# Optimization experiments

Hardware: AMD Instinct MI355X
Metric: run time of the kernel (lower is better)

The kernel has to match this reference:

```python
import jax, jax.numpy as jnp
import numpy as np

B, S, DIM = 2, 2048, 1024
EXPERT_DIM = 256
N_S, N_R, TOP_K = 2, 32, 4
EPS = 1e-6


def setup_inputs() -> dict:
    key = jax.random.key(0)
    ks = jax.random.split(key, 12)
    s1 = 1.0 / np.sqrt(DIM)        # fan-in init scale for Linear(dim, expert_dim)
    s2 = 1.0 / np.sqrt(EXPERT_DIM)  # fan-in init scale for Linear(expert_dim, dim)
    return {
        "x": jax.random.normal(ks[0], (B, S, DIM), jnp.float32),
        "rms_w": jnp.ones((DIM,), jnp.float32),
        "centroids": jax.random.normal(ks[1], (N_R, DIM), jnp.float32),
        # shared experts, stacked along leading expert axis
        "sW1": jax.random.normal(ks[2], (N_S, DIM, EXPERT_DIM), jnp.float32) * s1,
        "sb1": jax.random.normal(ks[3], (N_S, EXPERT_DIM), jnp.float32) * s1,
        "sW2": jax.random.normal(ks[4], (N_S, EXPERT_DIM, DIM), jnp.float32) * s2,
        "sb2": jax.random.normal(ks[5], (N_S, DIM), jnp.float32) * s2,
        # routed experts
        "rW1": jax.random.normal(ks[6], (N_R, DIM, EXPERT_DIM), jnp.float32) * s1,
        "rb1": jax.random.normal(ks[7], (N_R, EXPERT_DIM), jnp.float32) * s1,
        "rW2": jax.random.normal(ks[8], (N_R, EXPERT_DIM, DIM), jnp.float32) * s2,
        "rb2": jax.random.normal(ks[9], (N_R, DIM), jnp.float32) * s2,
    }


def _rmsnorm(x, w):
    xf = x.astype(jnp.float32)
    n = xf * jax.lax.rsqrt(jnp.mean(xf * xf, axis=-1, keepdims=True) + EPS)
    return w * n.astype(x.dtype)


def _experts(xf, W1, b1, W2, b2):
    # xf: [T, D]; W1: [E, D, H]; returns [E, T, D]
    # Expert = Sequential(Linear, Linear, GELU) -> gelu applied AFTER second linear
    h = jnp.einsum('td,edh->eth', xf, W1) + b1[:, None, :]
    o = jnp.einsum('eth,ehd->etd', h, W2) + b2[:, None, :]
    return jax.nn.gelu(o, approximate=False)


def reference(x, rms_w, centroids, sW1, sb1, sW2, sb2, rW1, rb1, rW2, rb2):
    xn = _rmsnorm(x, rms_w)                      # [B, S, D]
    xf = xn.reshape(-1, DIM)                     # [T, D]
    T = xf.shape[0]

    # shared experts: summed dense output
    shared = _experts(xf, sW1, sb1, sW2, sb2).sum(axis=0)   # [T, D]

    # routing
    affinity = jax.nn.softmax(xf @ centroids.T, axis=-1)    # [T, E]
    topk_scores, topk_idx = jax.lax.top_k(affinity, TOP_K)
    mask = jnp.zeros_like(affinity).at[jnp.arange(T)[:, None], topk_idx].set(topk_scores)

    # dense-compute-then-mask, faithful to original module
    routed_all = _experts(xf, rW1, rb1, rW2, rb2)           # [E, T, D]
    routed = jnp.einsum('te,etd->td', mask, routed_all)     # [T, D]

    y = xn + (shared + routed).reshape(B, S, DIM)
    return y, affinity
```

## Files before the change

### kernel.cpp

```cpp
#include <hip/hip_runtime.h>
#include <hip/hip_bf16.h>
#include <math.h>

#define T_TOK 4096
#define DIM   1024
#define HDIM  256
#define N_SH  2
#define N_RT  32
#define N_E   34
#define TOPK  4
#define TB    128
#define MAXPB 200
#define NSLOT 6
#define OSW   34

typedef short bf16x8 __attribute__((ext_vector_type(8)));
typedef float f32x4  __attribute__((ext_vector_type(4)));
typedef unsigned short u16x8 __attribute__((ext_vector_type(8)));

__device__ __forceinline__ ushort f2b(float v) {
    __hip_bfloat16 h = __float2bfloat16(v);
    return *reinterpret_cast<const ushort*>(&h);
}
__device__ __forceinline__ float b2f(ushort u) {
    unsigned int x = ((unsigned int)u) << 16;
    return __uint_as_float(x);
}
__device__ __forceinline__ float gelu_tanh(float x) {
    float z = 0.7978845608028654f * (x + 0.044715f * x * x * x);
    float e = __expf(2.0f * z);
    float t = 1.0f - 2.0f / (e + 1.0f);
    return 0.5f * x * (1.0f + t);
}

__device__ __forceinline__ void gload_lds16(const ushort* g, ushort* l) {
    __builtin_amdgcn_global_load_lds(
        (const __attribute__((address_space(1))) void*)g,
        (__attribute__((address_space(3))) void*)l,
        16, 0, 0);
}

#define SBAR() __builtin_amdgcn_sched_barrier(0)

template<int K, int N>
__global__ __launch_bounds__(256) void pack_weights(
    const float* __restrict__ srcS, const float* __restrict__ srcR,
    ushort* __restrict__ dst)
{
    const int e = blockIdx.y;
    const float* src = (e < N_SH) ? (srcS + (size_t)e * K * N)
                                  : (srcR + (size_t)(e - N_SH) * K * N);
    const int kt  = K / 32;
    const int k32 = blockIdx.x % kt;
    const int nc  = blockIdx.x / kt;
    const int tid = threadIdx.x;

    __shared__ ushort ls[32][137];

    #pragma unroll
    for (int it = 0; it < 4; ++it) {
        const int row = it * 8 + (tid >> 5);
        const int c4  = tid & 31;
        const float4 v = *(const float4*)(src + (size_t)(k32 * 32 + row) * N
                                          + nc * 128 + c4 * 4);
        ls[row][c4 * 4 + 0] = f2b(v.x);
        ls[row][c4 * 4 + 1] = f2b(v.y);
        ls[row][c4 * 4 + 2] = f2b(v.z);
        ls[row][c4 * 4 + 3] = f2b(v.w);
    }
    __syncthreads();

    #pragma unroll
    for (int it = 0; it < 2; ++it) {
        const int t8   = tid >> 5;
        const int lane = it * 32 + (tid & 31);
        const int l16 = lane & 15, lk = lane >> 4;
        u16x8 o;
        #pragma unroll
        for (int j = 0; j < 8; ++j)
            o[j] = ls[lk * 8 + j][t8 * 16 + l16];
        const size_t tile = (size_t)(nc * 8 + t8) * kt + k32;
        *(u16x8*)(dst + (size_t)e * K * N + tile * 512 + lane * 8) = o;
    }
}

__global__ __launch_bounds__(256) void rms_router_kernel(
    const float* __restrict__ x, const float* __restrict__ rms_w,
    const float* __restrict__ cent,
    ushort* __restrict__ xnb, float* __restrict__ aff_out,
    int* __restrict__ tk_e, float* __restrict__ sscore)
{
    const int t0  = blockIdx.x * 4;
    const int tid = threadIdx.x;
    const int wid = tid >> 6;
    const int lane = tid & 63;
    const int t = t0 + wid;

    __shared__ float xsh[4][DIM];
    __shared__ float logits[4][N_RT];

    float4 xv[4], wv[4];
    float ss = 0.f;
    #pragma unroll
    for (int q = 0; q < 4; ++q) {
        xv[q] = ((const float4*)(x + (size_t)t * DIM))[lane + 64 * q];
        ss += xv[q].x*xv[q].x + xv[q].y*xv[q].y + xv[q].z*xv[q].z + xv[q].w*xv[q].w;
    }
    #pragma unroll
    for (int o = 32; o > 0; o >>= 1) ss += __shfl_down(ss, o);
    const float rstd = rsqrtf(__shfl(ss, 0) * (1.0f / (float)DIM) + 1e-6f);

    #pragma unroll
    for (int q = 0; q < 4; ++q)
        wv[q] = ((const float4*)rms_w)[lane + 64 * q];

    #pragma unroll
    for (int q = 0; q < 4; ++q) {
        float4 nv;
        nv.x = xv[q].x * rstd * wv[q].x;
        nv.y = xv[q].y * rstd * wv[q].y;
        nv.z = xv[q].z * rstd * wv[q].z;
        nv.w = xv[q].w * rstd * wv[q].w;
        ushort4 xb = make_ushort4(f2b(nv.x), f2b(nv.y), f2b(nv.z), f2b(nv.w));
        ((ushort4*)(xnb + (size_t)t * DIM))[lane + 64 * q] = xb;
        ((float4*)xsh[wid])[lane + 64 * q] = nv;
    }
    __syncthreads();

    #pragma unroll
    for (int ei = 0; ei < 8; ++ei) {
        const int e = wid * 8 + ei;
        const float4* c4 = (const float4*)(cent + (size_t)e * DIM);
        float a0 = 0.f, a1 = 0.f, a2 = 0.f, a3 = 0.f;
        #pragma unroll
        for (int q = 0; q < 4; ++q) {
            const float4 cv = c4[lane + 64 * q];
            const float4 x0 = ((const float4*)xsh[0])[lane + 64 * q];
            const float4 x1 = ((const float4*)xsh[1])[lane + 64 * q];
            const float4 x2 = ((const float4*)xsh[2])[lane + 64 * q];
            const float4 x3 = ((const float4*)xsh[3])[lane + 64 * q];
            a0 += cv.x*x0.x + cv.y*x0.y + cv.z*x0.z + cv.w*x0.w;
            a1 += cv.x*x1.x + cv.y*x1.y + cv.z*x1.z + cv.w*x1.w;
            a2 += cv.x*x2.x + cv.y*x2.y + cv.z*x2.z + cv.w*x2.w;
            a3 += cv.x*x3.x + cv.y*x3.y + cv.z*x3.z + cv.w*x3.w;
        }
        #pragma unroll
        for (int o = 32; o > 0; o >>= 1) {
            a0 += __shfl_down(a0, o);
            a1 += __shfl_down(a1, o);
            a2 += __shfl_down(a2, o);
            a3 += __shfl_down(a3, o);
        }
        if (lane == 0) {
            logits[0][e] = a0; logits[1][e] = a1;
            logits[2][e] = a2; logits[3][e] = a3;
        }
    }
    __syncthreads();

    {
        float v = (lane < N_RT) ? logits[wid][lane] : -INFINITY;
        float m = v;
        #pragma unroll
        for (int o = 32; o > 0; o >>= 1) m = fmaxf(m, __shfl_xor(m, o));
        float p = (lane < N_RT) ? expf(v - m) : 0.f;
        float s = p;
        #pragma unroll
        for (int o = 32; o > 0; o >>= 1) s += __shfl_xor(s, o);
        const float a = p / s;
        if (lane < N_RT) aff_out[(size_t)t * N_RT + lane] = a;
        if (lane < N_SH) sscore[(size_t)t * NSLOT + lane] = 1.f;

        float vv = (lane < N_RT) ? a : -1.f;
        #pragma unroll
        for (int it = 0; it < TOPK; ++it) {
            float mx = vv;
            #pragma unroll
            for (int o = 32; o > 0; o >>= 1) mx = fmaxf(mx, __shfl_xor(mx, o));
            unsigned long long msk = __ballot(vv == mx);
            int sel = __ffsll((long long)msk) - 1;
            sel = (sel < 0) ? 0 : (sel & (N_RT - 1));
            if (lane == 0) {
                tk_e[(size_t)t * TOPK + it] = sel;
                sscore[(size_t)t * NSLOT + 2 + it] = mx;
            }
            if (lane == sel) vv = -1.f;
        }
    }
}

__global__ __launch_bounds__(64) void scatter_kernel(
    const int* __restrict__ tk_e, int* __restrict__ counts, int* __restrict__ lists)
{
    const int e    = blockIdx.x;
    const int lane = threadIdx.x;
    const unsigned long long lt = (1ull << lane) - 1ull;
    int base = 0;
    int* lst = lists + (size_t)e * T_TOK;
    for (int c = 0; c < T_TOK * TOPK; c += 256) {
        const int4 v = *(const int4*)(tk_e + c + lane * 4);
        const bool p0 = (v.x == e), p1 = (v.y == e), p2 = (v.z == e), p3 = (v.w == e);
        const unsigned long long m0 = __ballot(p0);
        const unsigned long long m1 = __ballot(p1);
        const unsigned long long m2 = __ballot(p2);
        const unsigned long long m3 = __ballot(p3);
        const int c0 = __popcll(m0), c1 = __popcll(m1), c2 = __popcll(m2);
        if (p0) lst[base + __popcll(m0 & lt)] = c + lane * 4 + 0;
        if (p1) lst[base + c0 + __popcll(m1 & lt)] = c + lane * 4 + 1;
        if (p2) lst[base + c0 + c1 + __popcll(m2 & lt)] = c + lane * 4 + 2;
        if (p3) lst[base + c0 + c1 + c2 + __popcll(m3 & lt)] = c + lane * 4 + 3;
        base += c0 + c1 + c2 + __popcll(m3);
    }
    if (lane == 0) counts[e] = base;
}

__global__ __launch_bounds__(256) void residual_init(
    const ushort* __restrict__ xnb, float* __restrict__ y)
{
    const int idx = blockIdx.x * 256 + threadIdx.x;
    const ushort4 xr = *(const ushort4*)(xnb + (size_t)idx * 4);
    float4 a;
    a.x = b2f(xr.x); a.y = b2f(xr.y); a.z = b2f(xr.z); a.w = b2f(xr.w);
    ((float4*)y)[idx] = a;
}

template<bool ATOMIC>
__global__ __launch_bounds__(512, 2) void moe_mfma(
    const ushort* __restrict__ xnb,
    const ushort* __restrict__ W1p, const ushort* __restrict__ W2p,
    const float* __restrict__ sb1, const float* __restrict__ sb2,
    const float* __restrict__ rb1, const float* __restrict__ rb2,
    const int* __restrict__ counts, const int* __restrict__ lists,
    const float* __restrict__ sscore,
    ushort* __restrict__ sbuf, float* __restrict__ y)
{
    const int bi  = blockIdx.x;
    const int tid = threadIdx.x;

    __shared__ int    toks[TB];
    __shared__ int    orow[TB];
    __shared__ float  tscs[TB];
    __shared__ ushort hlds[TB * HDIM];
    __shared__ ushort astage[3 * 4096];
    __shared__ ushort ostage[8 * 64 * OSW];

    int e_full;
    const float *b1, *b2;

    if (bi < 64) {
        e_full = bi >> 5;
        const int tile = bi & 31;
        if (tid < TB) {
            const int t = tile * TB + tid;
            toks[tid] = t;
            orow[tid] = ATOMIC ? t : t * NSLOT + e_full;
            tscs[tid] = 1.f;
        }
        b1 = sb1 + e_full * HDIM;  b2 = sb2 + e_full * DIM;
    } else {
        const int j = bi - 64;
        const int b = j & 7, pos = j >> 3;
        int e = -1, tile = 0, accum = 0;
        #pragma unroll
        for (int g = 0; g < 4; ++g) {
            const int eg = b + 8 * g;
            const int tg = (counts[eg] + TB - 1) / TB;
            if (e < 0 && pos < accum + tg) { e = eg; tile = pos - accum; }
            accum += tg;
        }
        if (e < 0) return;
        e_full = N_SH + e;
        const int cnt = counts[e];
        if (tid < TB) {
            const int idx = tile * TB + tid;
            if (idx < cnt) {
                const int lv = lists[(size_t)e * T_TOK + idx];
                const int t = (lv >> 2) & (T_TOK - 1);
                toks[tid] = t;
                orow[tid] = ATOMIC ? t : t * NSLOT + 2 + (lv & 3);
                tscs[tid] = ATOMIC ? sscore[(size_t)t * NSLOT + 2 + (lv & 3)] : 0.f;
            } else {
                toks[tid] = 0;
                orow[tid] = ATOMIC ? 0 : T_TOK * NSLOT;
                tscs[tid] = 0.f;
            }
        }
        b1 = rb1 + e * HDIM;  b2 = rb2 + e * DIM;
    }
    __syncthreads();

    const int w = tid >> 6, lane = tid & 63;
    const int l16 = lane & 15, lk = lane >> 4;
    const int mh = w >> 2;
    const int nq = w & 3;

    const ushort* W1e = W1p + (size_t)e_full * DIM * HDIM;
    const ushort* W2e = W2p + (size_t)e_full * HDIM * DIM;

    {
        const ushort* asrc = xnb + (size_t)toks[w * 16 + (lane >> 2)] * DIM
                             + (lane & 3) * 8;
        SBAR();
        gload_lds16(asrc,      astage + 0 * 4096 + w * 512);
        gload_lds16(asrc + 32, astage + 1 * 4096 + w * 512);
        SBAR();

        const ushort* bbase[4];
        #pragma unroll
        for (int ni = 0; ni < 4; ++ni)
            bbase[ni] = W1e + (size_t)((nq * 4 + ni) * 32) * 512 + lane * 8;

        f32x4 acc[4][4];
        #pragma unroll
        for (int mi = 0; mi < 4; ++mi)
            #pragma unroll
            for (int ni = 0; ni < 4; ++ni) acc[mi][ni] = (f32x4){0.f,0.f,0.f,0.f};

        bf16x8 bc[4];
        #pragma unroll
        for (int ni = 0; ni < 4; ++ni) bc[ni] = *(const bf16x8*)bbase[ni];

        asm volatile("s_waitcnt vmcnt(5)" ::: "memory");
        __builtin_amdgcn_s_barrier();
        SBAR();

        #pragma unroll 2
        for (int k32 = 0; k32 < 32; ++k32) {
            const int cur = k32 % 3;
            bf16x8 a[4], bn[4];
            #pragma unroll
            for (int mi = 0; mi < 4; ++mi) {
                const int tloc = mh * 64 + mi * 16 + l16;
                a[mi] = *(const bf16x8*)(astage + cur * 4096 + tloc * 32 + lk * 8);
            }
            if (k32 < 31) {
                #pragma unroll
                for (int ni = 0; ni < 4; ++ni)
                    bn[ni] = *(const bf16x8*)(bbase[ni] + (size_t)(k32 + 1) * 512);
            }
            #pragma unroll
            for (int ni = 0; ni < 4; ++ni)
                #pragma unroll
                for (int mi = 0; mi < 4; ++mi)
                    acc[mi][ni] = __builtin_amdgcn_mfma_f32_16x16x32_bf16(a[mi], bc[ni], acc[mi][ni], 0, 0, 0);
            if (k32 < 31) {
                #pragma unroll
                for (int ni = 0; ni < 4; ++ni) bc[ni] = bn[ni];
            }

            if (k32 < 30) {
                asm volatile("s_waitcnt lgkmcnt(0)" ::: "memory");
                SBAR();
                gload_lds16(asrc + (k32 + 2) * 32,
                            astage + ((k32 + 2) % 3) * 4096 + w * 512);
                SBAR();
                asm volatile("s_waitcnt vmcnt(5)" ::: "memory");
                __builtin_amdgcn_s_barrier();
                SBAR();
            } else if (k32 == 30) {
                asm volatile("s_waitcnt vmcnt(4)" ::: "memory");
                __builtin_amdgcn_s_barrier();
                SBAR();
            }
        }

        #pragma unroll
        for (int ni = 0; ni < 4; ++ni) {
            const int n = nq * 64 + ni * 16 + l16;
            const float bv = b1[n];
            #pragma unroll
            for (int mi = 0; mi < 4; ++mi) {
                #pragma unroll
                for (int r = 0; r < 4; ++r) {
                    const int m = mh * 64 + mi * 16 + lk * 4 + r;
                    const int byte = (m * (HDIM * 2) + n * 2) ^ ((m & 7) << 4);
                    *(ushort*)((char*)hlds + byte) = f2b(acc[mi][ni][r] + bv);
                }
            }
        }
    }
    __syncthreads();

    {
        for (int jc = 0; jc < 4; ++jc) {
            f32x4 acc2[4][4];
            #pragma unroll
            for (int mi = 0; mi < 4; ++mi)
                #pragma unroll
                for (int ni = 0; ni < 4; ++ni) acc2[mi][ni] = (f32x4){0.f,0.f,0.f,0.f};

            const ushort* b2base[4];
            #pragma unroll
            for (int ni = 0; ni < 4; ++ni)
                b2base[ni] = W2e + (size_t)((jc * 16 + nq * 4 + ni) * 8) * 512 + lane * 8;

            bf16x8 bc2[4];
            #pragma unroll
            for (int ni = 0; ni < 4; ++ni) bc2[ni] = *(const bf16x8*)b2base[ni];

            #pragma unroll
            for (int k32 = 0; k32 < 8; ++k32) {
                bf16x8 a2[4];
                #pragma unroll
                for (int mi = 0; mi < 4; ++mi) {
                    const int m = mh * 64 + mi * 16 + l16;
                    const int byte = (m * (HDIM * 2) + (k32 * 32 + lk * 8) * 2) ^ ((m & 7) << 4);
                    a2[mi] = *(const bf16x8*)((const char*)hlds + byte);
                }
                bf16x8 bn2[4];
                if (k32 < 7) {
                    #pragma unroll
                    for (int ni = 0; ni < 4; ++ni)
                        bn2[ni] = *(const bf16x8*)(b2base[ni] + (size_t)(k32 + 1) * 512);
                }
                #pragma unroll
                for (int ni = 0; ni < 4; ++ni)
                    #pragma unroll
                    for (int mi = 0; mi < 4; ++mi)
                        acc2[mi][ni] = __builtin_amdgcn_mfma_f32_16x16x32_bf16(a2[mi], bc2[ni], acc2[mi][ni], 0, 0, 0);
                if (k32 < 7) {
                    #pragma unroll
                    for (int ni = 0; ni < 4; ++ni) bc2[ni] = bn2[ni];
                }
            }

            if (ATOMIC) {
                #pragma unroll
                for (int ni = 0; ni < 4; ++ni) {
                    const int n = jc * 256 + nq * 64 + ni * 16 + l16;
                    const float bv = b2[n];
                    #pragma unroll
                    for (int mi = 0; mi < 4; ++mi)
                        #pragma unroll
                        for (int r = 0; r < 4; ++r) {
                            const int m = mi * 16 + lk * 4 + r;
                            const float val = gelu_tanh(acc2[mi][ni][r] + bv) * tscs[mh * 64 + m];
                            atomicAdd(&y[(size_t)orow[mh * 64 + m] * DIM + n], val);
                        }
                }
            } else {
                ushort* os = ostage + w * (64 * OSW);
                #pragma unroll
                for (int p = 0; p < 2; ++p) {
                    asm volatile("s_waitcnt lgkmcnt(0)" ::: "memory");
                    #pragma unroll
                    for (int q = 0; q < 2; ++q) {
                        const int ni = p * 2 + q;
                        const float bv = b2[jc * 256 + nq * 64 + ni * 16 + l16];
                        #pragma unroll
                        for (int mi = 0; mi < 4; ++mi)
                            #pragma unroll
                            for (int r = 0; r < 4; ++r) {
                                const int m = mi * 16 + lk * 4 + r;
                                os[m * OSW + q * 16 + l16] = f2b(acc2[mi][ni][r] + bv);
                            }
                    }
                    asm volatile("s_waitcnt lgkmcnt(0)" ::: "memory");
                    #pragma unroll
                    for (int rr = 0; rr < 4; ++rr) {
                        const int m  = rr * 16 + (lane >> 2);
                        const int nl = (lane & 3) * 8;
                        u16x8 vv = *(const u16x8*)(os + m * OSW + nl);
                        *(u16x8*)(sbuf + (size_t)orow[mh * 64 + m] * DIM
                                  + jc * 256 + nq * 64 + p * 32 + nl) = vv;
                    }
                }
            }
        }
    }
}

__global__ __launch_bounds__(256) void gather_kernel(
    const ushort* __restrict__ sbuf, const float* __restrict__ sscore,
    const ushort* __restrict__ xnb, float* __restrict__ y)
{
    const int idx = blockIdx.x * 256 + threadIdx.x;
    const int t = idx >> 8;
    const int d = (idx & 255) * 4;
    const ushort4 xr = *(const ushort4*)(xnb + (size_t)t * DIM + d);
    float4 a;
    a.x = b2f(xr.x); a.y = b2f(xr.y); a.z = b2f(xr.z); a.w = b2f(xr.w);
    #pragma unroll
    for (int s = 0; s < NSLOT; ++s) {
        const float sc = sscore[(size_t)t * NSLOT + s];
        const ushort4 u = *(const ushort4*)(sbuf + ((size_t)t * NSLOT + s) * DIM + d);
        a.x += gelu_tanh(b2f(u.x)) * sc;
        a.y += gelu_tanh(b2f(u.y)) * sc;
        a.z += gelu_tanh(b2f(u.z)) * sc;
        a.w += gelu_tanh(b2f(u.w)) * sc;
    }
    ((float4*)y)[idx] = a;
}

extern "C" void kernel_launch(void* const* d_in, const int* in_sizes, int n_in,
                              void* d_out, int out_size, void* d_ws, size_t ws_size,
                              hipStream_t stream) {
    const float* x      = (const float*)d_in[0];
    const float* rms_w  = (const float*)d_in[1];
    const float* cent   = (const float*)d_in[2];
    const float* sW1    = (const float*)d_in[3];
    const float* sb1    = (const float*)d_in[4];
    const float* sW2    = (const float*)d_in[5];
    const float* sb2    = (const float*)d_in[6];
    const float* rW1    = (const float*)d_in[7];
    const float* rb1    = (const float*)d_in[8];
    const float* rW2    = (const float*)d_in[9];
    const float* rb2    = (const float*)d_in[10];

    float* y_out   = (float*)d_out;
    float* aff_out = (float*)d_out + (size_t)T_TOK * DIM;

    char* p = (char*)d_ws;
    size_t off = 0;
    auto take = [&](size_t b) {
        char* r = p + off;
        off += (b + 255) & ~(size_t)255;
        return r;
    };
    ushort* xnb    = (ushort*)take((size_t)T_TOK * DIM * 2);
    ushort* W1p    = (ushort*)take((size_t)N_E * DIM * HDIM * 2);
    ushort* W2p    = (ushort*)take((size_t)N_E * HDIM * DIM * 2);
    int*    counts = (int*)take(N_RT * sizeof(int));
    int*    lists  = (int*)take((size_t)N_RT * T_TOK * 4);
    float*  sscore = (float*)take((size_t)T_TOK * NSLOT * 4);
    int*    tk_e   = (int*)take((size_t)T_TOK * TOPK * 4);
    ushort* sbuf   = (ushort*)take(((size_t)T_TOK * NSLOT + TB) * DIM * 2);
    const bool slot_ok = (off <= ws_size);

    pack_weights<DIM, HDIM><<<dim3(64, N_E), dim3(256), 0, stream>>>(sW1, rW1, W1p);
    pack_weights<HDIM, DIM><<<dim3(64, N_E), dim3(256), 0, stream>>>(sW2, rW2, W2p);

    rms_router_kernel<<<dim3(T_TOK / 4), dim3(256), 0, stream>>>(
        x, rms_w, cent, xnb, aff_out, tk_e, sscore);

    scatter_kernel<<<dim3(N_RT), dim3(64), 0, stream>>>(tk_e, counts, lists);

    const int grid = 64 + 8 * MAXPB;
    if (slot_ok) {
        moe_mfma<false><<<dim3(grid), dim3(512), 0, stream>>>(
            xnb, W1p, W2p, sb1, sb2, rb1, rb2, counts, lists,
            sscore, sbuf, y_out);
        gather_kernel<<<dim3((T_TOK * DIM / 4) / 256), dim3(256), 0, stream>>>(
            sbuf, sscore, xnb, y_out);
    } else {
        residual_init<<<dim3((T_TOK * DIM / 4) / 256), dim3(256), 0, stream>>>(
            xnb, y_out);
        moe_mfma<true><<<dim3(grid), dim3(512), 0, stream>>>(
            xnb, W1p, W2p, sb1, sb2, rb1, rb2, counts, lists,
            sscore, sbuf, y_out);
    }
}
```

Baseline: 140.0 us.

## Merge weight packing launches, batch 16 tokens per router block, parallelize scatter

Merges the two weight-pack launches into one grid using a z dimension. The router kernel now handles 16 tokens per block, so each centroid row load is reused across 16 tokens instead of 4. The scatter kernel splits the token scan across 4 waves with a two-pass count-then-write and a prefix over per-wave counts. The intent is to cut launch overhead and the latency of the small preprocessing kernels, at the cost of more registers in the router (16 accumulators) and fewer router blocks.

```diff
diff --git a/kernel.cpp b/kernel.cpp
--- a/kernel.cpp
+++ b/kernel.cpp
@@ -42,12 +42,18 @@
 
 #define SBAR() __builtin_amdgcn_sched_barrier(0)
 
-template<int K, int N>
 __global__ __launch_bounds__(256) void pack_weights(
-    const float* __restrict__ srcS, const float* __restrict__ srcR,
-    ushort* __restrict__ dst)
+    const float* __restrict__ sW1, const float* __restrict__ rW1,
+    const float* __restrict__ sW2, const float* __restrict__ rW2,
+    ushort* __restrict__ W1p, ushort* __restrict__ W2p)
 {
+    const int z = blockIdx.z;
+    const int K = z ? HDIM : DIM;
+    const int N = z ? DIM : HDIM;
     const int e = blockIdx.y;
+    const float* srcS = z ? sW2 : sW1;
+    const float* srcR = z ? rW2 : rW1;
+    ushort* dst       = z ? W2p : W1p;
     const float* src = (e < N_SH) ? (srcS + (size_t)e * K * N)
                                   : (srcR + (size_t)(e - N_SH) * K * N);
     const int kt  = K / 32;
@@ -90,40 +96,43 @@
     ushort* __restrict__ xnb, float* __restrict__ aff_out,
     int* __restrict__ tk_e, float* __restrict__ sscore)
 {
-    const int t0  = blockIdx.x * 4;
+    const int t0  = blockIdx.x * 16;
     const int tid = threadIdx.x;
     const int wid = tid >> 6;
     const int lane = tid & 63;
-    const int t = t0 + wid;
-
-    __shared__ float xsh[4][DIM];
-    __shared__ float logits[4][N_RT];
-
-    float4 xv[4], wv[4];
-    float ss = 0.f;
-    #pragma unroll
-    for (int q = 0; q < 4; ++q) {
-        xv[q] = ((const float4*)(x + (size_t)t * DIM))[lane + 64 * q];
-        ss += xv[q].x*xv[q].x + xv[q].y*xv[q].y + xv[q].z*xv[q].z + xv[q].w*xv[q].w;
-    }
-    #pragma unroll
-    for (int o = 32; o > 0; o >>= 1) ss += __shfl_down(ss, o);
-    const float rstd = rsqrtf(__shfl(ss, 0) * (1.0f / (float)DIM) + 1e-6f);
-
+
+    __shared__ float xsh[16][DIM];
+    __shared__ float logits[16][N_RT];
+
+    float4 wv4[4];
     #pragma unroll
     for (int q = 0; q < 4; ++q)
-        wv[q] = ((const float4*)rms_w)[lane + 64 * q];
-
-    #pragma unroll
-    for (int q = 0; q < 4; ++q) {
-        float4 nv;
-        nv.x = xv[q].x * rstd * wv[q].x;
-        nv.y = xv[q].y * rstd * wv[q].y;
-        nv.z = xv[q].z * rstd * wv[q].z;
-        nv.w = xv[q].w * rstd * wv[q].w;
-        ushort4 xb = make_ushort4(f2b(nv.x), f2b(nv.y), f2b(nv.z), f2b(nv.w));
-        ((ushort4*)(xnb + (size_t)t * DIM))[lane + 64 * q] = xb;
-        ((float4*)xsh[wid])[lane + 64 * q] = nv;
+        wv4[q] = ((const float4*)rms_w)[lane + 64 * q];
+
+    #pragma unroll
+    for (int j = 0; j < 4; ++j) {
+        const int t = t0 + wid * 4 + j;
+        float4 xv[4];
+        float ss = 0.f;
+        #pragma unroll
+        for (int q = 0; q < 4; ++q) {
+            xv[q] = ((const float4*)(x + (size_t)t * DIM))[lane + 64 * q];
+            ss += xv[q].x*xv[q].x + xv[q].y*xv[q].y + xv[q].z*xv[q].z + xv[q].w*xv[q].w;
+        }
+        #pragma unroll
+        for (int o = 32; o > 0; o >>= 1) ss += __shfl_down(ss, o);
+        const float rstd = rsqrtf(__shfl(ss, 0) * (1.0f / (float)DIM) + 1e-6f);
+        #pragma unroll
+        for (int q = 0; q < 4; ++q) {
+            float4 nv;
+            nv.x = xv[q].x * rstd * wv4[q].x;
+            nv.y = xv[q].y * rstd * wv4[q].y;
+            nv.z = xv[q].z * rstd * wv4[q].z;
+            nv.w = xv[q].w * rstd * wv4[q].w;
+            ushort4 xb = make_ushort4(f2b(nv.x), f2b(nv.y), f2b(nv.z), f2b(nv.w));
+            ((ushort4*)(xnb + (size_t)t * DIM))[lane + 64 * q] = xb;
+            ((float4*)xsh[wid * 4 + j])[lane + 64 * q] = nv;
+        }
     }
     __syncthreads();
 
@@ -131,35 +140,36 @@
     for (int ei = 0; ei < 8; ++ei) {
         const int e = wid * 8 + ei;
         const float4* c4 = (const float4*)(cent + (size_t)e * DIM);
-        float a0 = 0.f, a1 = 0.f, a2 = 0.f, a3 = 0.f;
+        float acc[16];
+        #pragma unroll
+        for (int tk = 0; tk < 16; ++tk) acc[tk] = 0.f;
         #pragma unroll
         for (int q = 0; q < 4; ++q) {
             const float4 cv = c4[lane + 64 * q];
-            const float4 x0 = ((const float4*)xsh[0])[lane + 64 * q];
-            const float4 x1 = ((const float4*)xsh[1])[lane + 64 * q];
-            const float4 x2 = ((const float4*)xsh[2])[lane + 64 * q];
-            const float4 x3 = ((const float4*)xsh[3])[lane + 64 * q];
-            a0 += cv.x*x0.x + cv.y*x0.y + cv.z*x0.z + cv.w*x0.w;
-            a1 += cv.x*x1.x + cv.y*x1.y + cv.z*x1.z + cv.w*x1.w;
-            a2 += cv.x*x2.x + cv.y*x2.y + cv.z*x2.z + cv.w*x2.w;
-            a3 += cv.x*x3.x + cv.y*x3.y + cv.z*x3.z + cv.w*x3.w;
+            #pragma unroll
+            for (int tk = 0; tk < 16; ++tk) {
+                const float4 xq = ((const float4*)xsh[tk])[lane + 64 * q];
+                acc[tk] += cv.x*xq.x + cv.y*xq.y + cv.z*xq.z + cv.w*xq.w;
+            }
         }
         #pragma unroll
         for (int o = 32; o > 0; o >>= 1) {
-            a0 += __shfl_down(a0, o);
-            a1 += __shfl_down(a1, o);
-            a2 += __shfl_down(a2, o);
-            a3 += __shfl_down(a3, o);
+            #pragma unroll
+            for (int tk = 0; tk < 16; ++tk)
+                acc[tk] += __shfl_down(acc[tk], o);
         }
         if (lane == 0) {
-            logits[0][e] = a0; logits[1][e] = a1;
-            logits[2][e] = a2; logits[3][e] = a3;
+            #pragma unroll
+            for (int tk = 0; tk < 16; ++tk) logits[tk][e] = acc[tk];
         }
     }
     __syncthreads();
 
-    {
-        float v = (lane < N_RT) ? logits[wid][lane] : -INFINITY;
+    #pragma unroll
+    for (int j = 0; j < 4; ++j) {
+        const int tk = wid * 4 + j;
+        const int t  = t0 + tk;
+        float v = (lane < N_RT) ? logits[tk][lane] : -INFINITY;
         float m = v;
         #pragma unroll
         for (int o = 32; o > 0; o >>= 1) m = fmaxf(m, __shfl_xor(m, o));
@@ -189,29 +199,51 @@
     }
 }
 
-__global__ __launch_bounds__(64) void scatter_kernel(
+__global__ __launch_bounds__(256) void scatter_kernel(
     const int* __restrict__ tk_e, int* __restrict__ counts, int* __restrict__ lists)
 {
     const int e    = blockIdx.x;
-    const int lane = threadIdx.x;
+    const int tid  = threadIdx.x;
+    const int wv   = tid >> 6;
+    const int lane = tid & 63;
     const unsigned long long lt = (1ull << lane) - 1ull;
+    const int CH = T_TOK * TOPK / 4;
+    const int base0 = wv * CH;
+
+    __shared__ int wcnt[4];
+
+    int cnt = 0;
+    for (int c = 0; c < CH; c += 256) {
+        const int4 v = *(const int4*)(tk_e + base0 + c + lane * 4);
+        cnt += __popcll(__ballot(v.x == e));
+        cnt += __popcll(__ballot(v.y == e));
+        cnt += __popcll(__ballot(v.z == e));
+        cnt += __popcll(__ballot(v.w == e));
+    }
+    if (lane == 0) wcnt[wv] = cnt;
+    __syncthreads();
+
     int base = 0;
+    #pragma unroll
+    for (int g = 0; g < 4; ++g)
+        if (g < wv) base += wcnt[g];
+
     int* lst = lists + (size_t)e * T_TOK;
-    for (int c = 0; c < T_TOK * TOPK; c += 256) {
-        const int4 v = *(const int4*)(tk_e + c + lane * 4);
+    for (int c = 0; c < CH; c += 256) {
+        const int4 v = *(const int4*)(tk_e + base0 + c + lane * 4);
         const bool p0 = (v.x == e), p1 = (v.y == e), p2 = (v.z == e), p3 = (v.w == e);
         const unsigned long long m0 = __ballot(p0);
         const unsigned long long m1 = __ballot(p1);
         const unsigned long long m2 = __ballot(p2);
         const unsigned long long m3 = __ballot(p3);
         const int c0 = __popcll(m0), c1 = __popcll(m1), c2 = __popcll(m2);
-        if (p0) lst[base + __popcll(m0 & lt)] = c + lane * 4 + 0;
-        if (p1) lst[base + c0 + __popcll(m1 & lt)] = c + lane * 4 + 1;
-        if (p2) lst[base + c0 + c1 + __popcll(m2 & lt)] = c + lane * 4 + 2;
-        if (p3) lst[base + c0 + c1 + c2 + __popcll(m3 & lt)] = c + lane * 4 + 3;
+        if (p0) lst[base + __popcll(m0 & lt)] = base0 + c + lane * 4 + 0;
+        if (p1) lst[base + c0 + __popcll(m1 & lt)] = base0 + c + lane * 4 + 1;
+        if (p2) lst[base + c0 + c1 + __popcll(m2 & lt)] = base0 + c + lane * 4 + 2;
+        if (p3) lst[base + c0 + c1 + c2 + __popcll(m3 & lt)] = base0 + c + lane * 4 + 3;
         base += c0 + c1 + c2 + __popcll(m3);
     }
-    if (lane == 0) counts[e] = base;
+    if (tid == 0) counts[e] = wcnt[0] + wcnt[1] + wcnt[2] + wcnt[3];
 }
 
 __global__ __launch_bounds__(256) void residual_init(
@@ -527,13 +559,13 @@
     ushort* sbuf   = (ushort*)take(((size_t)T_TOK * NSLOT + TB) * DIM * 2);
     const bool slot_ok = (off <= ws_size);
 
-    pack_weights<DIM, HDIM><<<dim3(64, N_E), dim3(256), 0, stream>>>(sW1, rW1, W1p);
-    pack_weights<HDIM, DIM><<<dim3(64, N_E), dim3(256), 0, stream>>>(sW2, rW2, W2p);
-
-    rms_router_kernel<<<dim3(T_TOK / 4), dim3(256), 0, stream>>>(
+    pack_weights<<<dim3(64, N_E, 2), dim3(256), 0, stream>>>(
+        sW1, rW1, sW2, rW2, W1p, W2p);
+
+    rms_router_kernel<<<dim3(T_TOK / 16), dim3(256), 0, stream>>>(
         x, rms_w, cent, xnb, aff_out, tk_e, sscore);
 
-    scatter_kernel<<<dim3(N_RT), dim3(64), 0, stream>>>(tk_e, counts, lists);
+    scatter_kernel<<<dim3(N_RT), dim3(256), 0, stream>>>(tk_e, counts, lists);
 
     const int grid = 64 + 8 * MAXPB;
     if (slot_ok) {
```

Result: faster. 128.3 us (-8.3%).
